# Kernel optimization log

Hardware: AMD Instinct MI355X
Metric: run time of the kernel (lower is better)

Reference implementation:

```python
import jax, jax.numpy as jnp
import numpy as np
import math

B, S, D = 16, 512, 1024
H, L = 16, 4
DH = D // H
EPS = 1e-5


def _layernorm(x, w, b):
    mu = jnp.mean(x, axis=-1, keepdims=True)
    var = jnp.mean(jnp.square(x - mu), axis=-1, keepdims=True)
    return (x - mu) / jnp.sqrt(var + EPS) * w + b


def _pos_encoding(s, d):
    pos = jnp.arange(s, dtype=jnp.float32)[:, None]                      # [s,1]
    div = jnp.exp(jnp.arange(0, d, 2, dtype=jnp.float32) * (-math.log(10000.0) / d))
    ang = pos * div[None, :]                                             # [s,d/2]
    return jnp.stack([jnp.sin(ang), jnp.cos(ang)], axis=-1).reshape(s, d)  # interleave sin/cos


def _attention_layer(x, Wq, bq, Wv, bv, Wo, bo, gamma, ln_w, ln_b, mask):
    bs, s, d = x.shape
    # q_linear == k_linear (kq_same=True)
    q = (x @ Wq.T + bq).reshape(bs, s, H, DH).transpose(0, 2, 1, 3)      # [b,h,s,dh]
    k = q
    v = (x @ Wv.T + bv).reshape(bs, s, H, DH).transpose(0, 2, 1, 3)

    scores = jnp.einsum('bhqd,bhkd->bhqk', q, k) / math.sqrt(DH)         # [b,h,s,s]

    # distance-decay modulation (dist_scores is detached in the original)
    p = jax.nn.softmax(jnp.where(mask, scores, -1e32), axis=-1)
    distcum = jnp.cumsum(p, axis=-1)
    disttot = jnp.sum(p, axis=-1, keepdims=True)
    idx = jnp.arange(s, dtype=jnp.float32)
    pos_eff = jnp.abs(idx[None, :] - idx[:, None])[None, None, :, :]     # |i-j|
    dist = jnp.sqrt(jnp.maximum((disttot - distcum) * pos_eff, 0.0))
    dist = jax.lax.stop_gradient(dist)

    g = -jnp.abs(gamma)[None, :, None, None]                             # [1,h,1,1]
    total_effect = jnp.clip(jnp.exp(dist * g), 1e-5, 1e5)
    scores = scores * total_effect

    scores = jnp.where(mask, scores, -1e32)
    attn = jax.nn.softmax(scores, axis=-1)
    attn = jnp.where(mask, attn, 0.0)

    # maxout=True (peek_cur=False): clamp(1/max, max=5)
    scale = jnp.minimum(1.0 / jnp.max(attn, axis=-1, keepdims=True), 5.0)
    attn = attn * scale

    out = jnp.einsum('bhqk,bhkd->bhqd', attn, v)                         # [b,h,s,dh]
    out = out.transpose(0, 2, 1, 3).reshape(bs, s, d)
    out = out @ Wo.T + bo

    # eval mode: dropout = identity; residual + layernorm
    return _layernorm(x + out, ln_w, ln_b), attn


def reference(x, lens, Wq, bq, Wv, bv, Wo, bo, gammas, ln_w, ln_b, fln_w, fln_b):
    del lens  # only used in training-mode random masking
    s = x.shape[1]
    q = x + _pos_encoding(s, D)[None, :, :]
    mask = jnp.tril(jnp.ones((s, s), dtype=bool), -1)[None, None, :, :]  # peek_cur=False
    scores = None
    for l in range(L):
        q, scores = _attention_layer(q, Wq[l], bq[l], Wv[l], bv[l], Wo[l], bo[l],
                                     gammas[l], ln_w[l], ln_b[l], mask)
    return _layernorm(q, fln_w, fln_b), scores


def setup_inputs() -> dict:
    key = jax.random.key(0)
    ks = jax.random.split(key, 8)
    wscale = 1.0 / math.sqrt(D)
    return {
        'x': jax.random.normal(ks[0], (B, S, D), dtype=jnp.float32),
        'lens': jax.random.randint(ks[1], (B,), 1, S),
        'Wq': jax.random.normal(ks[2], (L, D, D), dtype=jnp.float32) * wscale,
        'bq': jnp.zeros((L, D), dtype=jnp.float32),
        'Wv': jax.random.normal(ks[3], (L, D, D), dtype=jnp.float32) * wscale,
        'bv': jnp.zeros((L, D), dtype=jnp.float32),
        'Wo': jax.random.normal(ks[4], (L, D, D), dtype=jnp.float32) * wscale,
        'bo': jnp.zeros((L, D), dtype=jnp.float32),
        'gammas': jax.random.uniform(ks[5], (L, H), dtype=jnp.float32, minval=-1.7, maxval=1.7),
        'ln_w': jnp.ones((L, D), dtype=jnp.float32),
        'ln_b': jnp.zeros((L, D), dtype=jnp.float32),
        'fln_w': jnp.ones((D,), dtype=jnp.float32),
        'fln_b': jnp.zeros((D,), dtype=jnp.float32),
    }
```

## Files before the change

kernel.cpp:

```cpp
#include <hip/hip_runtime.h>
#include <hip/hip_bf16.h>

#define BB 16
#define SS 512
#define DD 1024
#define HH 16
#define LL 4
#define DHH 64
#define GK 1024

typedef __attribute__((ext_vector_type(8))) short short8;
typedef __attribute__((ext_vector_type(4))) float f32x4;
typedef __attribute__((ext_vector_type(8))) _Float16 half8;

__device__ __forceinline__ unsigned short f2bf(float f) {
  union { float f; unsigned int u; } v; v.f = f;
  unsigned int r = v.u + 0x7FFFu + ((v.u >> 16) & 1u);
  return (unsigned short)(r >> 16);
}
__device__ __forceinline__ float bf2f(unsigned short u) {
  union { unsigned int i; float f; } v; v.i = ((unsigned)u) << 16; return v.f;
}

__device__ __forceinline__ float wave_max(float v) {
#pragma unroll
  for (int off = 32; off > 0; off >>= 1) v = fmaxf(v, __shfl_xor(v, off));
  return v;
}
__device__ __forceinline__ float wave_sum(float v) {
#pragma unroll
  for (int off = 32; off > 0; off >>= 1) v += __shfl_xor(v, off);
  return v;
}
__device__ __forceinline__ float half_max(float v) {
#pragma unroll
  for (int off = 16; off > 0; off >>= 1) v = fmaxf(v, __shfl_xor(v, off));
  return v;
}
__device__ __forceinline__ float half_sum(float v) {
#pragma unroll
  for (int off = 16; off > 0; off >>= 1) v += __shfl_xor(v, off);
  return v;
}

__device__ __forceinline__ void gl16(const void* g, void* l) {
  __builtin_amdgcn_global_load_lds(
      (const __attribute__((address_space(1))) unsigned int*)(uintptr_t)g,
      (__attribute__((address_space(3))) unsigned int*)(unsigned int)(uintptr_t)l,
      16, 0, 0);
}

__global__ __launch_bounds__(256) void k_w2bf_all(
    const float* __restrict__ wq, const float* __restrict__ wv,
    const float* __restrict__ wo, unsigned short* __restrict__ oqv,
    unsigned short* __restrict__ oo) {
  size_t i4 = ((size_t)blockIdx.x * 256 + threadIdx.x) * 4;
  const size_t QV = (size_t)2 * LL * DD * DD;
  const float* src;
  unsigned short* dst;
  if (i4 < QV) {
    size_t l = i4 >> 21;
    size_t r = i4 & ((1u << 21) - 1);
    src = (r < (1u << 20)) ? wq + (l << 20) + r
                           : wv + (l << 20) + (r - (1u << 20));
    dst = oqv + i4;
  } else {
    size_t j = i4 - QV;
    src = wo + j;
    dst = oo + j;
  }
  float4 v = *(const float4*)src;
  uint2 pk;
  pk.x = (unsigned)f2bf(v.x) | ((unsigned)f2bf(v.y) << 16);
  pk.y = (unsigned)f2bf(v.z) | ((unsigned)f2bf(v.w) << 16);
  *(uint2*)dst = pk;
}

__global__ __launch_bounds__(256) void k_add_pe(const float* __restrict__ x,
                                                unsigned short* __restrict__ outb) {
  size_t i4 = ((size_t)blockIdx.x * 256 + threadIdx.x) * 4;
  int d0 = (int)(i4 & (DD - 1));
  int s = (int)((i4 >> 10) & (SS - 1));
  float4 xv = *(const float4*)(x + i4);
  int ip0 = d0 >> 1;
  float f0 = __expf((float)ip0 * -0.017988946039016f);
  float f1 = __expf((float)(ip0 + 1) * -0.017988946039016f);
  float s0v, c0v, s1v, c1v;
  __sincosf((float)s * f0, &s0v, &c0v);
  __sincosf((float)s * f1, &s1v, &c1v);
  float o0 = xv.x + s0v, o1 = xv.y + c0v, o2 = xv.z + s1v, o3 = xv.w + c1v;
  uint2 pk;
  pk.x = (unsigned)f2bf(o0) | ((unsigned)f2bf(o1) << 16);
  pk.y = (unsigned)f2bf(o2) | ((unsigned)f2bf(o3) << 16);
  *(uint2*)(outb + i4) = pk;
}

template <int MODE>
__global__ __launch_bounds__(256) void k_gemm(
    const unsigned short* __restrict__ A, const unsigned short* __restrict__ W,
    const float* __restrict__ bias, const float* __restrict__ bias2,
    void* __restrict__ out, void* __restrict__ out2) {
  __shared__ unsigned short As[2][128 * 32];
  __shared__ unsigned short Bs[2][128 * 32];
  const int tid = threadIdx.x;
  const int lane = tid & 63;
  const int w = tid >> 6;
  const int wr = w >> 1, wc = w & 1;
  const int fr = lane & 15, fq = lane >> 4;

  int bid = blockIdx.x;
  const int cpx = gridDim.x >> 3;
  bid = (bid & 7) * cpx + (bid >> 3);
  const int bm = (bid & 63) * 128;
  const int bn = (bid >> 6) * 128;

  f32x4 acc[4][4] = {};

  const unsigned short* ga = A + (size_t)(bm + w * 16 + (lane >> 2)) * GK + (lane & 3) * 8;
  const unsigned short* gb = W + (size_t)(bn + w * 16 + (lane >> 2)) * GK + (lane & 3) * 8;

  auto STAGE = [&](int buf, int k0) {
    unsigned short* la = As[buf] + w * 512;
    unsigned short* lb = Bs[buf] + w * 512;
    gl16(ga + k0, la);
    gl16(ga + 64 * GK + k0, la + 2048);
    gl16(gb + k0, lb);
    gl16(gb + 64 * GK + k0, lb + 2048);
  };

  STAGE(0, 0);
  __syncthreads();
  int cur = 0;
  for (int k0 = 0; k0 < GK; k0 += 32) {
    if (k0 + 32 < GK) STAGE(cur ^ 1, k0 + 32);
    short8 af[4], bf[4];
#pragma unroll
    for (int m = 0; m < 4; ++m)
      af[m] = *(const short8*)(As[cur] + (wr * 64 + m * 16 + fr) * 32 + fq * 8);
#pragma unroll
    for (int n = 0; n < 4; ++n)
      bf[n] = *(const short8*)(Bs[cur] + (wc * 64 + n * 16 + fr) * 32 + fq * 8);
#pragma unroll
    for (int m = 0; m < 4; ++m)
#pragma unroll
      for (int n = 0; n < 4; ++n)
        acc[m][n] = __builtin_amdgcn_mfma_f32_16x16x32_bf16(af[m], bf[n], acc[m][n], 0, 0, 0);
    __syncthreads();
    cur ^= 1;
  }

#pragma unroll
  for (int m = 0; m < 4; ++m) {
    const int row0 = bm + wr * 64 + m * 16 + fq * 4;
#pragma unroll
    for (int n = 0; n < 4; ++n) {
      const int col = bn + wc * 64 + n * 16 + fr;
      if constexpr (MODE == 0) {
        const float bsv = bias[col];
        unsigned short* o = (unsigned short*)out;
#pragma unroll
        for (int r = 0; r < 4; ++r)
          o[(size_t)(row0 + r) * DD + col] = f2bf(acc[m][n][r] + bsv);
      } else {
        if (col < DD) {
          const float bsv = bias[col];
          unsigned short* o = (unsigned short*)out;
#pragma unroll
          for (int r = 0; r < 4; ++r)
            o[(size_t)(row0 + r) * DD + col] = f2bf(acc[m][n][r] + bsv);
        } else {
          const int c2 = col - DD;
          const float bsv = bias2[c2];
          unsigned short* o = (unsigned short*)out2;
          const int bi = row0 >> 9, si = row0 & (SS - 1);
          uint2 pk;
          pk.x = (unsigned)f2bf(acc[m][n][0] + bsv) | ((unsigned)f2bf(acc[m][n][1] + bsv) << 16);
          pk.y = (unsigned)f2bf(acc[m][n][2] + bsv) | ((unsigned)f2bf(acc[m][n][3] + bsv) << 16);
          *(uint2*)(o + ((size_t)bi * DD + c2) * SS + si) = pk;
        }
      }
    }
  }
}

__global__ __launch_bounds__(512) void k_attn(
    const unsigned short* __restrict__ Q, const unsigned short* __restrict__ Vt,
    const float* __restrict__ gam, unsigned short* __restrict__ AO,
    float* __restrict__ scores_out) {
  __shared__ _Float16 sc_s[64][520];
  __shared__ unsigned short KV[64][72];

  const int tid = threadIdx.x;
  const int lane = tid & 63;
  const int w = tid >> 6;
  const int wr = w & 3;
  const int wc = w >> 2;
  const int fr = lane & 15, fq = lane >> 4;

  const int itile = 7 - (blockIdx.x >> 8);
  const int bh = blockIdx.x & 255;
  const int b = bh >> 4;
  const int h = bh & 15;
  const int i0 = itile * 64;
  const int njt = itile + 1;
  const int jcap = njt * 64;

  const unsigned short* Qb = Q + (size_t)b * SS * DD + h * DHH;
  const unsigned short* Vtb = Vt + ((size_t)b * DD + h * DHH) * SS;
  const float gneg = -fabsf(gam[h]);

  const int srow = tid >> 3;
  const int sdb = (tid & 7) * 8;

  const unsigned short* qrow = Qb + (size_t)(i0 + wr * 16 + fr) * DD;
  short8 a0 = *(const short8*)(qrow + fq * 8);
  short8 a1 = *(const short8*)(qrow + 32 + fq * 8);

  short8 kreg = *(const short8*)(Qb + (size_t)srow * DD + sdb);
  for (int jt = 0; jt < njt; ++jt) {
    *(short8*)&KV[srow][sdb] = kreg;
    const unsigned short* nsrc = (jt + 1 < njt)
        ? Qb + (size_t)((jt + 1) * 64 + srow) * DD + sdb
        : Vtb + (size_t)srow * SS + sdb;
    kreg = *(const short8*)nsrc;
    __syncthreads();

    short8 b00 = *(const short8*)&KV[wc * 32 + fr][fq * 8];
    short8 b01 = *(const short8*)&KV[wc * 32 + fr][32 + fq * 8];
    short8 b10 = *(const short8*)&KV[wc * 32 + 16 + fr][fq * 8];
    short8 b11 = *(const short8*)&KV[wc * 32 + 16 + fr][32 + fq * 8];
    f32x4 s0 = {}, s1 = {};
    __builtin_amdgcn_s_setprio(1);
    s0 = __builtin_amdgcn_mfma_f32_16x16x32_bf16(a0, b00, s0, 0, 0, 0);
    s0 = __builtin_amdgcn_mfma_f32_16x16x32_bf16(a1, b01, s0, 0, 0, 0);
    s1 = __builtin_amdgcn_mfma_f32_16x16x32_bf16(a0, b10, s1, 0, 0, 0);
    s1 = __builtin_amdgcn_mfma_f32_16x16x32_bf16(a1, b11, s1, 0, 0, 0);
    __builtin_amdgcn_s_setprio(0);

#pragma unroll
    for (int n = 0; n < 2; ++n) {
      const int j = jt * 64 + wc * 32 + n * 16 + fr;
#pragma unroll
      for (int r = 0; r < 4; ++r) {
        const int row = wr * 16 + fq * 4 + r;
        const float val = (n ? s1[r] : s0[r]) * 0.125f;
        sc_s[row][j] = (j < i0 + row) ? (_Float16)val : (_Float16)(-65504.0f);
      }
    }
    __syncthreads();
  }
  *(short8*)&KV[srow][sdb] = kreg;

  if (itile >= 4) {
    const int jb = lane << 3;
#pragma unroll 2
    for (int q = 0; q < 8; ++q) {
      const int r_i = w * 8 + q;
      const int gi = i0 + r_i;
      half8 hv = *(const half8*)(&sc_s[r_i][0] + jb);
      float sc[8];
#pragma unroll
      for (int c = 0; c < 8; ++c) sc[c] = (float)hv[c];
#pragma unroll
      for (int c = 0; c < 8; ++c)
        if (jb + c >= jcap) sc[c] = -1e30f;

      float p[8];
      float lsum = 0.0f;
#pragma unroll
      for (int c = 0; c < 8; ++c) {
        p[c] = __expf(sc[c]);
        lsum += p[c];
      }

      float xs = lsum;
#pragma unroll
      for (int off = 1; off < 64; off <<= 1) {
        float y = __shfl_up(xs, off);
        if (lane >= off) xs += y;
      }
      const float tot = __shfl(xs, 63);
      const float inv = 1.0f / tot;
      float run = xs - lsum;

      float s2[8];
#pragma unroll
      for (int c = 0; c < 8; ++c) {
        run += p[c];
        float cum = run * inv;
        float dist = sqrtf(fmaxf((1.0f - cum) * (float)(gi - (jb + c)), 0.0f));
        float te = __expf(gneg * dist);
        te = fminf(fmaxf(te, 1e-5f), 1e5f);
        s2[c] = sc[c] * te;
      }

      float m2 = s2[0];
#pragma unroll
      for (int c = 1; c < 8; ++c) m2 = fmaxf(m2, s2[c]);
      m2 = wave_max(m2);
      float e[8];
      float lsum2 = 0.0f;
#pragma unroll
      for (int c = 0; c < 8; ++c) {
        e[c] = __expf(s2[c] - m2);
        lsum2 += e[c];
      }
      float tot2 = wave_sum(lsum2);
      float mult = fminf(tot2, 5.0f) / tot2;

      float av[8];
#pragma unroll
      for (int c = 0; c < 8; ++c) av[c] = (gi == 0) ? 0.0f : e[c] * mult;

      if (scores_out) {
        float* so = scores_out + ((size_t)(b * HH + h) * SS + gi) * SS + jb;
        *(float4*)(so) = make_float4(av[0], av[1], av[2], av[3]);
        *(float4*)(so + 4) = make_float4(av[4], av[5], av[6], av[7]);
      }

      short8 pk;
#pragma unroll
      for (int c = 0; c < 8; ++c) pk[c] = (short)f2bf(av[c]);
      *(short8*)((unsigned short*)&sc_s[r_i][0] + jb) = pk;
    }
  } else {
    const int half = lane >> 5;
    const int ll = lane & 31;
    const int jb = ll << 3;
    for (int q = 0; q < 4; ++q) {
      const int r_i = w * 8 + q * 2 + half;
      const int gi = i0 + r_i;
      half8 hv = *(const half8*)(&sc_s[r_i][0] + jb);
      float sc[8];
#pragma unroll
      for (int c = 0; c < 8; ++c) sc[c] = (float)hv[c];
#pragma unroll
      for (int c = 0; c < 8; ++c)
        if (jb + c >= jcap) sc[c] = -1e30f;

      float p[8];
      float lsum = 0.0f;
#pragma unroll
      for (int c = 0; c < 8; ++c) {
        p[c] = __expf(sc[c]);
        lsum += p[c];
      }

      float xs = lsum;
#pragma unroll
      for (int off = 1; off < 32; off <<= 1) {
        float y = __shfl_up(xs, off, 32);
        if (ll >= off) xs += y;
      }
      const float tot = __shfl(xs, 31, 32);
      const float inv = 1.0f / tot;
      float run = xs - lsum;

      float s2[8];
#pragma unroll
      for (int c = 0; c < 8; ++c) {
        run += p[c];
        float cum = run * inv;
        float dist = sqrtf(fmaxf((1.0f - cum) * (float)(gi - (jb + c)), 0.0f));
        float te = __expf(gneg * dist);
        te = fminf(fmaxf(te, 1e-5f), 1e5f);
        s2[c] = sc[c] * te;
      }

      float m2 = s2[0];
#pragma unroll
      for (int c = 1; c < 8; ++c) m2 = fmaxf(m2, s2[c]);
      m2 = half_max(m2);
      float e[8];
      float lsum2 = 0.0f;
#pragma unroll
      for (int c = 0; c < 8; ++c) {
        e[c] = __expf(s2[c] - m2);
        lsum2 += e[c];
      }
      const float tot2 = half_sum(lsum2);
      const float mult = fminf(tot2, 5.0f) / tot2;

      float av[8];
#pragma unroll
      for (int c = 0; c < 8; ++c) av[c] = (gi == 0) ? 0.0f : e[c] * mult;

      if (scores_out) {
        float* so = scores_out + ((size_t)(b * HH + h) * SS + gi) * SS + jb;
        *(float4*)(so) = make_float4(av[0], av[1], av[2], av[3]);
        *(float4*)(so + 4) = make_float4(av[4], av[5], av[6], av[7]);
        *(float4*)(so + 256) = make_float4(0.f, 0.f, 0.f, 0.f);
        *(float4*)(so + 260) = make_float4(0.f, 0.f, 0.f, 0.f);
      }

      short8 pk;
#pragma unroll
      for (int c = 0; c < 8; ++c) pk[c] = (short)f2bf(av[c]);
      *(short8*)((unsigned short*)&sc_s[r_i][0] + jb) = pk;
    }
  }
  __syncthreads();

  short8 vreg;
  if (njt > 1) vreg = *(const short8*)(Vtb + (size_t)srow * SS + 64 + sdb);
  f32x4 o0 = {}, o1 = {};
  for (int jt = 0; jt < njt; ++jt) {
    const unsigned short* arow = (const unsigned short*)&sc_s[wr * 16 + fr][0];
    short8 pa0 = *(const short8*)(arow + jt * 64 + fq * 8);
    short8 pa1 = *(const short8*)(arow + jt * 64 + 32 + fq * 8);
    short8 c00 = *(const short8*)&KV[wc * 32 + fr][fq * 8];
    short8 c01 = *(const short8*)&KV[wc * 32 + fr][32 + fq * 8];
    short8 c10 = *(const short8*)&KV[wc * 32 + 16 + fr][fq * 8];
    short8 c11 = *(const short8*)&KV[wc * 32 + 16 + fr][32 + fq * 8];
    __builtin_amdgcn_s_setprio(1);
    o0 = __builtin_amdgcn_mfma_f32_16x16x32_bf16(pa0, c00, o0, 0, 0, 0);
    o0 = __builtin_amdgcn_mfma_f32_16x16x32_bf16(pa1, c01, o0, 0, 0, 0);
    o1 = __builtin_amdgcn_mfma_f32_16x16x32_bf16(pa0, c10, o1, 0, 0, 0);
    o1 = __builtin_amdgcn_mfma_f32_16x16x32_bf16(pa1, c11, o1, 0, 0, 0);
    __builtin_amdgcn_s_setprio(0);
    __syncthreads();
    if (jt + 1 < njt) {
      *(short8*)&KV[srow][sdb] = vreg;
      if (jt + 2 < njt) vreg = *(const short8*)(Vtb + (size_t)srow * SS + (jt + 2) * 64 + sdb);
      __syncthreads();
    }
  }

#pragma unroll
  for (int n = 0; n < 2; ++n) {
    const int d = h * DHH + wc * 32 + n * 16 + fr;
#pragma unroll
    for (int r = 0; r < 4; ++r) {
      const int row = i0 + wr * 16 + fq * 4 + r;
      AO[((size_t)b * SS + row) * DD + d] = f2bf(n ? o1[r] : o0[r]);
    }
  }
}

__global__ __launch_bounds__(256) void k_res_ln(
    const unsigned short* __restrict__ x, const unsigned short* __restrict__ r,
    const float* __restrict__ w, const float* __restrict__ b,
    unsigned short* __restrict__ outb, float* __restrict__ outf) {
  __shared__ float red[4];
  const int row = blockIdx.x;
  const int tid = threadIdx.x;
  const int lane = tid & 63, wv = tid >> 6;
  uint2 xa = ((const uint2*)(x + (size_t)row * DD))[tid];
  float y0 = bf2f((unsigned short)xa.x);
  float y1 = bf2f((unsigned short)(xa.x >> 16));
  float y2 = bf2f((unsigned short)xa.y);
  float y3 = bf2f((unsigned short)(xa.y >> 16));
  if (r) {
    uint2 ra = ((const uint2*)(r + (size_t)row * DD))[tid];
    y0 += bf2f((unsigned short)ra.x);
    y1 += bf2f((unsigned short)(ra.x >> 16));
    y2 += bf2f((unsigned short)ra.y);
    y3 += bf2f((unsigned short)(ra.y >> 16));
  }
  float s = y0 + y1 + y2 + y3;
  s = wave_sum(s);
  if (lane == 0) red[wv] = s;
  __syncthreads();
  float mean = (red[0] + red[1] + red[2] + red[3]) * (1.0f / DD);
  __syncthreads();
  float d0 = y0 - mean, d1 = y1 - mean, d2 = y2 - mean, d3 = y3 - mean;
  float s2 = d0 * d0 + d1 * d1 + d2 * d2 + d3 * d3;
  s2 = wave_sum(s2);
  if (lane == 0) red[wv] = s2;
  __syncthreads();
  float var = (red[0] + red[1] + red[2] + red[3]) * (1.0f / DD);
  float rstd = rsqrtf(var + 1e-5f);
  float4 ww = ((const float4*)w)[tid];
  float4 bb = ((const float4*)b)[tid];
  float o0 = d0 * rstd * ww.x + bb.x;
  float o1 = d1 * rstd * ww.y + bb.y;
  float o2 = d2 * rstd * ww.z + bb.z;
  float o3 = d3 * rstd * ww.w + bb.w;
  if (outf) {
    ((float4*)(outf + (size_t)row * DD))[tid] = make_float4(o0, o1, o2, o3);
  } else {
    uint2 pk;
    pk.x = (unsigned)f2bf(o0) | ((unsigned)f2bf(o1) << 16);
    pk.y = (unsigned)f2bf(o2) | ((unsigned)f2bf(o3) << 16);
    ((uint2*)(outb + (size_t)row * DD))[tid] = pk;
  }
}

extern "C" void kernel_launch(void* const* d_in, const int* in_sizes, int n_in,
                              void* d_out, int out_size, void* d_ws, size_t ws_size,
                              hipStream_t stream) {
  (void)in_sizes; (void)n_in; (void)out_size; (void)ws_size;
  const float* x = (const float*)d_in[0];
  const float* Wq = (const float*)d_in[2];
  const float* bq = (const float*)d_in[3];
  const float* Wv = (const float*)d_in[4];
  const float* bv = (const float*)d_in[5];
  const float* Wo = (const float*)d_in[6];
  const float* bo = (const float*)d_in[7];
  const float* gam = (const float*)d_in[8];
  const float* lnw = (const float*)d_in[9];
  const float* lnb = (const float*)d_in[10];
  const float* flnw = (const float*)d_in[11];
  const float* flnb = (const float*)d_in[12];

  float* out0 = (float*)d_out;
  float* scores = out0 + (size_t)BB * SS * DD;
  const size_t BUF = (size_t)BB * SS * DD;
  const size_t WSZ = (size_t)LL * DD * DD;
  const size_t BHSS = (size_t)BB * HH * SS * SS;

  unsigned short* us = (unsigned short*)d_ws;
  unsigned short* Abf0 = us;
  unsigned short* Abf1 = us + BUF;
  unsigned short* Qbf = us + 2 * BUF;
  unsigned short* VtB = us + 3 * BUF;
  unsigned short* AObf = us + 4 * BUF;
  unsigned short* Pb = us + 5 * BUF;
  unsigned short* Wob = us + 6 * BUF;
  unsigned short* Wqvb = (unsigned short*)scores + (2 * BHSS - 2 * WSZ);

  const int M = BB * SS;

  k_w2bf_all<<<dim3(3 * WSZ / 1024), 256, 0, stream>>>(Wq, Wv, Wo, Wqvb, Wob);
  k_add_pe<<<dim3(BUF / 1024), 256, 0, stream>>>(x, Abf0);

  unsigned short* Acur = Abf0;
  unsigned short* Anx = Abf1;
  for (int l = 0; l < LL; ++l) {
    float* sc_dst = (l == LL - 1) ? scores : nullptr;
    k_gemm<3><<<dim3(1024), 256, 0, stream>>>(Acur, Wqvb + (size_t)l * 2048 * DD,
                                              bq + l * DD, bv + l * DD, Qbf, VtB);
    k_attn<<<dim3(BB * HH * 8), 512, 0, stream>>>(Qbf, VtB, gam + l * HH, AObf, sc_dst);
    k_gemm<0><<<dim3(512), 256, 0, stream>>>(AObf, Wob + (size_t)l * DD * DD,
                                             bo + l * DD, nullptr, Pb, nullptr);
    k_res_ln<<<dim3(M), 256, 0, stream>>>(Acur, Pb, lnw + l * DD, lnb + l * DD, Anx, nullptr);
    unsigned short* t = Acur; Acur = Anx; Anx = t;
  }
  k_res_ln<<<dim3(M), 256, 0, stream>>>(Acur, nullptr, flnw, flnb, nullptr, out0);
}
```

Measured before the change: 786.7 us.

## Pair causal query tiles per attention block and merge softmax reductions

```diff
diff --git a/kernel.cpp b/kernel.cpp
--- a/kernel.cpp
+++ b/kernel.cpp
@@ -197,13 +197,10 @@
   const int wc = w >> 2;
   const int fr = lane & 15, fq = lane >> 4;
 
-  const int itile = 7 - (blockIdx.x >> 8);
+  const int pair = blockIdx.x >> 8;
   const int bh = blockIdx.x & 255;
   const int b = bh >> 4;
   const int h = bh & 15;
-  const int i0 = itile * 64;
-  const int njt = itile + 1;
-  const int jcap = njt * 64;
 
   const unsigned short* Qb = Q + (size_t)b * SS * DD + h * DHH;
   const unsigned short* Vtb = Vt + ((size_t)b * DD + h * DHH) * SS;
@@ -212,227 +209,233 @@
   const int srow = tid >> 3;
   const int sdb = (tid & 7) * 8;
 
-  const unsigned short* qrow = Qb + (size_t)(i0 + wr * 16 + fr) * DD;
-  short8 a0 = *(const short8*)(qrow + fq * 8);
-  short8 a1 = *(const short8*)(qrow + 32 + fq * 8);
-
-  short8 kreg = *(const short8*)(Qb + (size_t)srow * DD + sdb);
-  for (int jt = 0; jt < njt; ++jt) {
+  for (int it2 = 0; it2 < 2; ++it2) {
+    const int itile = it2 == 0 ? 7 - pair : pair;
+    const int i0 = itile * 64;
+    const int njt = itile + 1;
+    const int jcap = njt * 64;
+    if (it2 == 1) __syncthreads();
+
+    const unsigned short* qrow = Qb + (size_t)(i0 + wr * 16 + fr) * DD;
+    short8 a0 = *(const short8*)(qrow + fq * 8);
+    short8 a1 = *(const short8*)(qrow + 32 + fq * 8);
+
+    short8 kreg = *(const short8*)(Qb + (size_t)srow * DD + sdb);
+    for (int jt = 0; jt < njt; ++jt) {
+      *(short8*)&KV[srow][sdb] = kreg;
+      const unsigned short* nsrc = (jt + 1 < njt)
+          ? Qb + (size_t)((jt + 1) * 64 + srow) * DD + sdb
+          : Vtb + (size_t)srow * SS + sdb;
+      kreg = *(const short8*)nsrc;
+      __syncthreads();
+
+      short8 b00 = *(const short8*)&KV[wc * 32 + fr][fq * 8];
+      short8 b01 = *(const short8*)&KV[wc * 32 + fr][32 + fq * 8];
+      short8 b10 = *(const short8*)&KV[wc * 32 + 16 + fr][fq * 8];
+      short8 b11 = *(const short8*)&KV[wc * 32 + 16 + fr][32 + fq * 8];
+      f32x4 s0 = {}, s1 = {};
+      __builtin_amdgcn_s_setprio(1);
+      s0 = __builtin_amdgcn_mfma_f32_16x16x32_bf16(a0, b00, s0, 0, 0, 0);
+      s0 = __builtin_amdgcn_mfma_f32_16x16x32_bf16(a1, b01, s0, 0, 0, 0);
+      s1 = __builtin_amdgcn_mfma_f32_16x16x32_bf16(a0, b10, s1, 0, 0, 0);
+      s1 = __builtin_amdgcn_mfma_f32_16x16x32_bf16(a1, b11, s1, 0, 0, 0);
+      __builtin_amdgcn_s_setprio(0);
+
+#pragma unroll
+      for (int n = 0; n < 2; ++n) {
+        const int j = jt * 64 + wc * 32 + n * 16 + fr;
+#pragma unroll
+        for (int r = 0; r < 4; ++r) {
+          const int row = wr * 16 + fq * 4 + r;
+          const float val = (n ? s1[r] : s0[r]) * 0.125f;
+          sc_s[row][j] = (j < i0 + row) ? (_Float16)val : (_Float16)(-65504.0f);
+        }
+      }
+      __syncthreads();
+    }
     *(short8*)&KV[srow][sdb] = kreg;
-    const unsigned short* nsrc = (jt + 1 < njt)
-        ? Qb + (size_t)((jt + 1) * 64 + srow) * DD + sdb
-        : Vtb + (size_t)srow * SS + sdb;
-    kreg = *(const short8*)nsrc;
-    __syncthreads();
-
-    short8 b00 = *(const short8*)&KV[wc * 32 + fr][fq * 8];
-    short8 b01 = *(const short8*)&KV[wc * 32 + fr][32 + fq * 8];
-    short8 b10 = *(const short8*)&KV[wc * 32 + 16 + fr][fq * 8];
-    short8 b11 = *(const short8*)&KV[wc * 32 + 16 + fr][32 + fq * 8];
-    f32x4 s0 = {}, s1 = {};
-    __builtin_amdgcn_s_setprio(1);
-    s0 = __builtin_amdgcn_mfma_f32_16x16x32_bf16(a0, b00, s0, 0, 0, 0);
-    s0 = __builtin_amdgcn_mfma_f32_16x16x32_bf16(a1, b01, s0, 0, 0, 0);
-    s1 = __builtin_amdgcn_mfma_f32_16x16x32_bf16(a0, b10, s1, 0, 0, 0);
-    s1 = __builtin_amdgcn_mfma_f32_16x16x32_bf16(a1, b11, s1, 0, 0, 0);
-    __builtin_amdgcn_s_setprio(0);
-
-#pragma unroll
-    for (int n = 0; n < 2; ++n) {
-      const int j = jt * 64 + wc * 32 + n * 16 + fr;
-#pragma unroll
-      for (int r = 0; r < 4; ++r) {
-        const int row = wr * 16 + fq * 4 + r;
-        const float val = (n ? s1[r] : s0[r]) * 0.125f;
-        sc_s[row][j] = (j < i0 + row) ? (_Float16)val : (_Float16)(-65504.0f);
+
+    if (itile >= 4) {
+      const int jb = lane << 3;
+#pragma unroll 2
+      for (int q = 0; q < 8; ++q) {
+        const int r_i = w * 8 + q;
+        const int gi = i0 + r_i;
+        half8 hv = *(const half8*)(&sc_s[r_i][0] + jb);
+        float sc[8];
+#pragma unroll
+        for (int c = 0; c < 8; ++c) sc[c] = (float)hv[c];
+#pragma unroll
+        for (int c = 0; c < 8; ++c)
+          if (jb + c >= jcap) sc[c] = -1e30f;
+
+        float p[8];
+        float lsum = 0.0f;
+#pragma unroll
+        for (int c = 0; c < 8; ++c) {
+          p[c] = __expf(sc[c]);
+          lsum += p[c];
+        }
+
+        float xs = lsum;
+#pragma unroll
+        for (int off = 1; off < 64; off <<= 1) {
+          float y = __shfl_up(xs, off);
+          if (lane >= off) xs += y;
+        }
+        const float tot = __shfl(xs, 63);
+        const float inv = 1.0f / tot;
+        float run = xs - lsum;
+
+        float s2[8];
+        float m2l = -3e38f;
+#pragma unroll
+        for (int c = 0; c < 8; ++c) {
+          run += p[c];
+          float cum = run * inv;
+          float dist = sqrtf(fmaxf((1.0f - cum) * (float)(gi - (jb + c)), 0.0f));
+          float te = __expf(gneg * dist);
+          te = fminf(fmaxf(te, 1e-5f), 1e5f);
+          s2[c] = sc[c] * te;
+          m2l = fmaxf(m2l, s2[c]);
+        }
+        float e[8];
+        float ls2 = 0.0f;
+#pragma unroll
+        for (int c = 0; c < 8; ++c) {
+          e[c] = __expf(s2[c]);
+          ls2 += e[c];
+        }
+        const float m2 = wave_max(m2l);
+        const float tot2 = wave_sum(ls2);
+        const float rr = tot2 * __expf(-m2);
+        const float mult = fminf(rr, 5.0f) / tot2;
+
+        float av[8];
+#pragma unroll
+        for (int c = 0; c < 8; ++c) av[c] = (gi == 0) ? 0.0f : e[c] * mult;
+
+        if (scores_out) {
+          float* so = scores_out + ((size_t)(b * HH + h) * SS + gi) * SS + jb;
+          *(float4*)(so) = make_float4(av[0], av[1], av[2], av[3]);
+          *(float4*)(so + 4) = make_float4(av[4], av[5], av[6], av[7]);
+        }
+
+        short8 pk;
+#pragma unroll
+        for (int c = 0; c < 8; ++c) pk[c] = (short)f2bf(av[c]);
+        *(short8*)((unsigned short*)&sc_s[r_i][0] + jb) = pk;
+      }
+    } else {
+      const int half = lane >> 5;
+      const int ll = lane & 31;
+      const int jb = ll << 3;
+      for (int q = 0; q < 4; ++q) {
+        const int r_i = w * 8 + q * 2 + half;
+        const int gi = i0 + r_i;
+        half8 hv = *(const half8*)(&sc_s[r_i][0] + jb);
+        float sc[8];
+#pragma unroll
+        for (int c = 0; c < 8; ++c) sc[c] = (float)hv[c];
+#pragma unroll
+        for (int c = 0; c < 8; ++c)
+          if (jb + c >= jcap) sc[c] = -1e30f;
+
+        float p[8];
+        float lsum = 0.0f;
+#pragma unroll
+        for (int c = 0; c < 8; ++c) {
+          p[c] = __expf(sc[c]);
+          lsum += p[c];
+        }
+
+        float xs = lsum;
+#pragma unroll
+        for (int off = 1; off < 32; off <<= 1) {
+          float y = __shfl_up(xs, off, 32);
+          if (ll >= off) xs += y;
+        }
+        const float tot = __shfl(xs, 31, 32);
+        const float inv = 1.0f / tot;
+        float run = xs - lsum;
+
+        float s2[8];
+        float m2l = -3e38f;
+#pragma unroll
+        for (int c = 0; c < 8; ++c) {
+          run += p[c];
+          float cum = run * inv;
+          float dist = sqrtf(fmaxf((1.0f - cum) * (float)(gi - (jb + c)), 0.0f));
+          float te = __expf(gneg * dist);
+          te = fminf(fmaxf(te, 1e-5f), 1e5f);
+          s2[c] = sc[c] * te;
+          m2l = fmaxf(m2l, s2[c]);
+        }
+        float e[8];
+        float ls2 = 0.0f;
+#pragma unroll
+        for (int c = 0; c < 8; ++c) {
+          e[c] = __expf(s2[c]);
+          ls2 += e[c];
+        }
+        const float m2 = half_max(m2l);
+        const float tot2 = half_sum(ls2);
+        const float rr = tot2 * __expf(-m2);
+        const float mult = fminf(rr, 5.0f) / tot2;
+
+        float av[8];
+#pragma unroll
+        for (int c = 0; c < 8; ++c) av[c] = (gi == 0) ? 0.0f : e[c] * mult;
+
+        if (scores_out) {
+          float* so = scores_out + ((size_t)(b * HH + h) * SS + gi) * SS + jb;
+          *(float4*)(so) = make_float4(av[0], av[1], av[2], av[3]);
+          *(float4*)(so + 4) = make_float4(av[4], av[5], av[6], av[7]);
+          *(float4*)(so + 256) = make_float4(0.f, 0.f, 0.f, 0.f);
+          *(float4*)(so + 260) = make_float4(0.f, 0.f, 0.f, 0.f);
+        }
+
+        short8 pk;
+#pragma unroll
+        for (int c = 0; c < 8; ++c) pk[c] = (short)f2bf(av[c]);
+        *(short8*)((unsigned short*)&sc_s[r_i][0] + jb) = pk;
       }
     }
     __syncthreads();
-  }
-  *(short8*)&KV[srow][sdb] = kreg;
-
-  if (itile >= 4) {
-    const int jb = lane << 3;
-#pragma unroll 2
-    for (int q = 0; q < 8; ++q) {
-      const int r_i = w * 8 + q;
-      const int gi = i0 + r_i;
-      half8 hv = *(const half8*)(&sc_s[r_i][0] + jb);
-      float sc[8];
-#pragma unroll
-      for (int c = 0; c < 8; ++c) sc[c] = (float)hv[c];
-#pragma unroll
-      for (int c = 0; c < 8; ++c)
-        if (jb + c >= jcap) sc[c] = -1e30f;
-
-      float p[8];
-      float lsum = 0.0f;
-#pragma unroll
-      for (int c = 0; c < 8; ++c) {
-        p[c] = __expf(sc[c]);
-        lsum += p[c];
+
+    short8 vreg;
+    if (njt > 1) vreg = *(const short8*)(Vtb + (size_t)srow * SS + 64 + sdb);
+    f32x4 o0 = {}, o1 = {};
+    for (int jt = 0; jt < njt; ++jt) {
+      const unsigned short* arow = (const unsigned short*)&sc_s[wr * 16 + fr][0];
+      short8 pa0 = *(const short8*)(arow + jt * 64 + fq * 8);
+      short8 pa1 = *(const short8*)(arow + jt * 64 + 32 + fq * 8);
+      short8 c00 = *(const short8*)&KV[wc * 32 + fr][fq * 8];
+      short8 c01 = *(const short8*)&KV[wc * 32 + fr][32 + fq * 8];
+      short8 c10 = *(const short8*)&KV[wc * 32 + 16 + fr][fq * 8];
+      short8 c11 = *(const short8*)&KV[wc * 32 + 16 + fr][32 + fq * 8];
+      __builtin_amdgcn_s_setprio(1);
+      o0 = __builtin_amdgcn_mfma_f32_16x16x32_bf16(pa0, c00, o0, 0, 0, 0);
+      o0 = __builtin_amdgcn_mfma_f32_16x16x32_bf16(pa1, c01, o0, 0, 0, 0);
+      o1 = __builtin_amdgcn_mfma_f32_16x16x32_bf16(pa0, c10, o1, 0, 0, 0);
+      o1 = __builtin_amdgcn_mfma_f32_16x16x32_bf16(pa1, c11, o1, 0, 0, 0);
+      __builtin_amdgcn_s_setprio(0);
+      __syncthreads();
+      if (jt + 1 < njt) {
+        *(short8*)&KV[srow][sdb] = vreg;
+        if (jt + 2 < njt) vreg = *(const short8*)(Vtb + (size_t)srow * SS + (jt + 2) * 64 + sdb);
+        __syncthreads();
       }
-
-      float xs = lsum;
-#pragma unroll
-      for (int off = 1; off < 64; off <<= 1) {
-        float y = __shfl_up(xs, off);
-        if (lane >= off) xs += y;
+    }
+
+#pragma unroll
+    for (int n = 0; n < 2; ++n) {
+      const int d = h * DHH + wc * 32 + n * 16 + fr;
+#pragma unroll
+      for (int r = 0; r < 4; ++r) {
+        const int row = i0 + wr * 16 + fq * 4 + r;
+        AO[((size_t)b * SS + row) * DD + d] = f2bf(n ? o1[r] : o0[r]);
       }
-      const float tot = __shfl(xs, 63);
-      const float inv = 1.0f / tot;
-      float run = xs - lsum;
-
-      float s2[8];
-#pragma unroll
-      for (int c = 0; c < 8; ++c) {
-        run += p[c];
-        float cum = run * inv;
-        float dist = sqrtf(fmaxf((1.0f - cum) * (float)(gi - (jb + c)), 0.0f));
-        float te = __expf(gneg * dist);
-        te = fminf(fmaxf(te, 1e-5f), 1e5f);
-        s2[c] = sc[c] * te;
-      }
-
-      float m2 = s2[0];
-#pragma unroll
-      for (int c = 1; c < 8; ++c) m2 = fmaxf(m2, s2[c]);
-      m2 = wave_max(m2);
-      float e[8];
-      float lsum2 = 0.0f;
-#pragma unroll
-      for (int c = 0; c < 8; ++c) {
-        e[c] = __expf(s2[c] - m2);
-        lsum2 += e[c];
-      }
-      float tot2 = wave_sum(lsum2);
-      float mult = fminf(tot2, 5.0f) / tot2;
-
-      float av[8];
-#pragma unroll
-      for (int c = 0; c < 8; ++c) av[c] = (gi == 0) ? 0.0f : e[c] * mult;
-
-      if (scores_out) {
-        float* so = scores_out + ((size_t)(b * HH + h) * SS + gi) * SS + jb;
-        *(float4*)(so) = make_float4(av[0], av[1], av[2], av[3]);
-        *(float4*)(so + 4) = make_float4(av[4], av[5], av[6], av[7]);
-      }
-
-      short8 pk;
-#pragma unroll
-      for (int c = 0; c < 8; ++c) pk[c] = (short)f2bf(av[c]);
-      *(short8*)((unsigned short*)&sc_s[r_i][0] + jb) = pk;
-    }
-  } else {
-    const int half = lane >> 5;
-    const int ll = lane & 31;
-    const int jb = ll << 3;
-    for (int q = 0; q < 4; ++q) {
-      const int r_i = w * 8 + q * 2 + half;
-      const int gi = i0 + r_i;
-      half8 hv = *(const half8*)(&sc_s[r_i][0] + jb);
-      float sc[8];
-#pragma unroll
-      for (int c = 0; c < 8; ++c) sc[c] = (float)hv[c];
-#pragma unroll
-      for (int c = 0; c < 8; ++c)
-        if (jb + c >= jcap) sc[c] = -1e30f;
-
-      float p[8];
-      float lsum = 0.0f;
-#pragma unroll
-      for (int c = 0; c < 8; ++c) {
-        p[c] = __expf(sc[c]);
-        lsum += p[c];
-      }
-
-      float xs = lsum;
-#pragma unroll
-      for (int off = 1; off < 32; off <<= 1) {
-        float y = __shfl_up(xs, off, 32);
-        if (ll >= off) xs += y;
-      }
-      const float tot = __shfl(xs, 31, 32);
-      const float inv = 1.0f / tot;
-      float run = xs - lsum;
-
-      float s2[8];
-#pragma unroll
-      for (int c = 0; c < 8; ++c) {
-        run += p[c];
-        float cum = run * inv;
-        float dist = sqrtf(fmaxf((1.0f - cum) * (float)(gi - (jb + c)), 0.0f));
-        float te = __expf(gneg * dist);
-        te = fminf(fmaxf(te, 1e-5f), 1e5f);
-        s2[c] = sc[c] * te;
-      }
-
-      float m2 = s2[0];
-#pragma unroll
-      for (int c = 1; c < 8; ++c) m2 = fmaxf(m2, s2[c]);
-      m2 = half_max(m2);
-      float e[8];
-      float lsum2 = 0.0f;
-#pragma unroll
-      for (int c = 0; c < 8; ++c) {
-        e[c] = __expf(s2[c] - m2);
-        lsum2 += e[c];
-      }
-      const float tot2 = half_sum(lsum2);
-      const float mult = fminf(tot2, 5.0f) / tot2;
-
-      float av[8];
-#pragma unroll
-      for (int c = 0; c < 8; ++c) av[c] = (gi == 0) ? 0.0f : e[c] * mult;
-
-      if (scores_out) {
-        float* so = scores_out + ((size_t)(b * HH + h) * SS + gi) * SS + jb;
-        *(float4*)(so) = make_float4(av[0], av[1], av[2], av[3]);
-        *(float4*)(so + 4) = make_float4(av[4], av[5], av[6], av[7]);
-        *(float4*)(so + 256) = make_float4(0.f, 0.f, 0.f, 0.f);
-        *(float4*)(so + 260) = make_float4(0.f, 0.f, 0.f, 0.f);
-      }
-
-      short8 pk;
-#pragma unroll
-      for (int c = 0; c < 8; ++c) pk[c] = (short)f2bf(av[c]);
-      *(short8*)((unsigned short*)&sc_s[r_i][0] + jb) = pk;
-    }
-  }
-  __syncthreads();
-
-  short8 vreg;
-  if (njt > 1) vreg = *(const short8*)(Vtb + (size_t)srow * SS + 64 + sdb);
-  f32x4 o0 = {}, o1 = {};
-  for (int jt = 0; jt < njt; ++jt) {
-    const unsigned short* arow = (const unsigned short*)&sc_s[wr * 16 + fr][0];
-    short8 pa0 = *(const short8*)(arow + jt * 64 + fq * 8);
-    short8 pa1 = *(const short8*)(arow + jt * 64 + 32 + fq * 8);
-    short8 c00 = *(const short8*)&KV[wc * 32 + fr][fq * 8];
-    short8 c01 = *(const short8*)&KV[wc * 32 + fr][32 + fq * 8];
-    short8 c10 = *(const short8*)&KV[wc * 32 + 16 + fr][fq * 8];
-    short8 c11 = *(const short8*)&KV[wc * 32 + 16 + fr][32 + fq * 8];
-    __builtin_amdgcn_s_setprio(1);
-    o0 = __builtin_amdgcn_mfma_f32_16x16x32_bf16(pa0, c00, o0, 0, 0, 0);
-    o0 = __builtin_amdgcn_mfma_f32_16x16x32_bf16(pa1, c01, o0, 0, 0, 0);
-    o1 = __builtin_amdgcn_mfma_f32_16x16x32_bf16(pa0, c10, o1, 0, 0, 0);
-    o1 = __builtin_amdgcn_mfma_f32_16x16x32_bf16(pa1, c11, o1, 0, 0, 0);
-    __builtin_amdgcn_s_setprio(0);
-    __syncthreads();
-    if (jt + 1 < njt) {
-      *(short8*)&KV[srow][sdb] = vreg;
-      if (jt + 2 < njt) vreg = *(const short8*)(Vtb + (size_t)srow * SS + (jt + 2) * 64 + sdb);
-      __syncthreads();
-    }
-  }
-
-#pragma unroll
-  for (int n = 0; n < 2; ++n) {
-    const int d = h * DHH + wc * 32 + n * 16 + fr;
-#pragma unroll
-    for (int r = 0; r < 4; ++r) {
-      const int row = i0 + wr * 16 + fq * 4 + r;
-      AO[((size_t)b * SS + row) * DD + d] = f2bf(n ? o1[r] : o0[r]);
     }
   }
 }
@@ -530,7 +533,7 @@
     float* sc_dst = (l == LL - 1) ? scores : nullptr;
     k_gemm<3><<<dim3(1024), 256, 0, stream>>>(Acur, Wqvb + (size_t)l * 2048 * DD,
                                               bq + l * DD, bv + l * DD, Qbf, VtB);
-    k_attn<<<dim3(BB * HH * 8), 512, 0, stream>>>(Qbf, VtB, gam + l * HH, AObf, sc_dst);
+    k_attn<<<dim3(BB * HH * 4), 512, 0, stream>>>(Qbf, VtB, gam + l * HH, AObf, sc_dst);
     k_gemm<0><<<dim3(512), 256, 0, stream>>>(AObf, Wob + (size_t)l * DD * DD,
                                              bo + l * DD, nullptr, Pb, nullptr);
     k_res_ln<<<dim3(M), 256, 0, stream>>>(Acur, Pb, lnw + l * DD, lnb + l * DD, Anx, nullptr);
```

After: 812.3 us. 3.3% more time.
